# Optimization experiments

Measured on AMD Instinct MI355X. Metric: run time of the kernel, lower is better.

The kernel has to match this reference:

```python
import jax, jax.numpy as jnp
import numpy as np

B, S, D = 2, 2048, 1024
H = 16
DK = D // H
SCALE = 1.0 / np.sqrt(DK)

def setup_inputs() -> dict:
    key = jax.random.key(0)
    ks = jax.random.split(key, 11)
    std = 1.0 / np.sqrt(D)
    return {
        "query": jax.random.normal(ks[0], (B, S, D), jnp.float32),
        "key":   jax.random.normal(ks[1], (B, S, D), jnp.float32),
        "value": jax.random.normal(ks[2], (B, S, D), jnp.float32),
        "Wq": jax.random.normal(ks[3], (D, H * DK), jnp.float32) * std,
        "bq": jnp.zeros((H * DK,), jnp.float32),
        "Wk": jax.random.normal(ks[4], (D, H * DK), jnp.float32) * std,
        "bk": jnp.zeros((H * DK,), jnp.float32),
        "Wv": jax.random.normal(ks[5], (D, H * DK), jnp.float32) * std,
        "bv": jnp.zeros((H * DK,), jnp.float32),
        "Wo": jax.random.normal(ks[6], (D, D), jnp.float32) * std,
        "bo": jnp.zeros((D,), jnp.float32),
    }

def reference(query, key, value, Wq, bq, Wk, bk, Wv, bv, Wo, bo):
    b, s, _ = query.shape
    # projections -> [b, s, h, d_k]
    q = (query @ Wq + bq).reshape(b, s, H, DK)
    k = (key   @ Wk + bk).reshape(b, s, H, DK)
    v = (value @ Wv + bv).reshape(b, s, H, DK)
    # scores [b, i, j, h]
    scores = jnp.einsum('bihd,bjhd->bijh', q, k) * SCALE
    attn = jax.nn.softmax(scores, axis=2)  # softmax over key dim j
    # dropout rate 0.0 (eval mode) -> identity
    x = jnp.einsum('bijh,bjhd->bihd', attn, v).reshape(b, s, H * DK)
    return x @ Wo + bo
```

## Files before the change

### kernel.cpp

```cpp
#include <hip/hip_runtime.h>
#include <hip/hip_bf16.h>
#include <math.h>
#include <stdint.h>

constexpr int Bb = 2, Ss = 2048, Dd = 1024, Hh = 16;
constexpr int Mm = Bb * Ss;
constexpr int Nn = Dd;
constexpr int Kk = Dd;
constexpr float QSCALE = 0.125f * 1.44269504088896340736f;

typedef unsigned short ushort_t;
typedef __attribute__((ext_vector_type(8))) short bf16x8;
typedef __attribute__((ext_vector_type(4))) float f32x4;

#if __has_builtin(__builtin_amdgcn_exp2f)
#define EXP2F(x) __builtin_amdgcn_exp2f(x)
#else
#define EXP2F(x) exp2f(x)
#endif

__device__ __forceinline__ ushort_t f2bf(float f) {
  union { float f; unsigned u; } v; v.f = f;
  return (ushort_t)((v.u + 0x7fff + ((v.u >> 16) & 1)) >> 16);
}

__device__ __forceinline__ void load16_lds(const void* g, void* l) {
  __builtin_amdgcn_global_load_lds(
      (const __attribute__((address_space(1))) void*)(uintptr_t)g,
      (__attribute__((address_space(3))) void*)(uint32_t)(uintptr_t)l, 16, 0, 0);
}

__global__ __launch_bounds__(256) void prep(
    const float* __restrict__ q, const float* __restrict__ k,
    const float* __restrict__ v, ushort_t* __restrict__ qkvb,
    const float* __restrict__ Wq, const float* __restrict__ Wk,
    const float* __restrict__ Wv, const float* __restrict__ Wo,
    ushort_t* __restrict__ Wt) {
  const int bid = blockIdx.x;
  const int tid = threadIdx.x;
  if (bid < 12288) {
    const int z = bid >> 12, xi = bid & 4095;
    const float* src = (z == 0) ? q : (z == 1) ? k : v;
    ushort_t* dst = qkvb + (size_t)z * Mm * Kk;
    const size_t idx = ((size_t)xi * 256 + tid) * 4;
    const float4 val = *(const float4*)(src + idx);
    ushort4 o;
    o.x = f2bf(val.x); o.y = f2bf(val.y); o.z = f2bf(val.z); o.w = f2bf(val.w);
    *(ushort4*)(dst + idx) = o;
    return;
  }
  const int bid2 = bid - 12288;
  const int z = bid2 >> 8, rem = bid2 & 255;
  const float* W = (z == 0) ? Wq : (z == 1) ? Wk : (z == 2) ? Wv : Wo;
  ushort_t* out = Wt + (size_t)z * Kk * Nn;
  __shared__ float t[64][65];
  const int n0 = (rem & 15) * 64, k0 = (rem >> 4) * 64;
  const int lr = tid >> 4, lc = (tid & 15) * 4;
#pragma unroll
  for (int i = 0; i < 4; i++) {
    const int r = lr + i * 16;
    const float4 vv = *(const float4*)(W + (size_t)(k0 + r) * Nn + n0 + lc);
    t[r][lc] = vv.x; t[r][lc + 1] = vv.y; t[r][lc + 2] = vv.z; t[r][lc + 3] = vv.w;
  }
  __syncthreads();
  const int n = tid >> 2, kc = (tid & 3) * 16;
  ushort_t tmp[16];
#pragma unroll
  for (int j = 0; j < 16; j++) tmp[j] = f2bf(t[kc + j][n]);
  ushort_t* op = out + (size_t)(n0 + n) * Kk + k0 + kc;
  ((uint4*)op)[0] = ((uint4*)tmp)[0];
  ((uint4*)op)[1] = ((uint4*)tmp)[1];
}

__global__ __launch_bounds__(256) void transpose_v(
    const ushort_t* __restrict__ Vp, ushort_t* __restrict__ Vt) {
  __shared__ ushort_t t[64][68];
  const int tid = threadIdx.x;
  const int s0 = blockIdx.x * 64, h = blockIdx.y, b = blockIdx.z;
  const int lr = tid >> 4, lc = (tid & 15) * 4;
#pragma unroll
  for (int i = 0; i < 4; i++) {
    const int r = lr + i * 16;
    const ushort4 v =
        *(const ushort4*)(Vp + (size_t)(b * Ss + s0 + r) * Dd + h * 64 + lc);
    *(ushort4*)&t[r][lc] = v;
  }
  __syncthreads();
  const int d = tid >> 2, sc = (tid & 3) * 16;
  ushort_t tmp[16];
#pragma unroll
  for (int j = 0; j < 16; j++) tmp[j] = t[sc + j][d];
  ushort_t* op = Vt + ((size_t)b * Dd + h * 64 + d) * Ss + s0 + sc;
  ((uint4*)op)[0] = ((uint4*)tmp)[0];
  ((uint4*)op)[1] = ((uint4*)tmp)[1];
}

template <int BN, bool OUT_BF16>
__global__ __launch_bounds__(256) void gemm_mfma(
    const ushort_t* __restrict__ Abase, size_t a_stride,
    const ushort_t* __restrict__ Wbase, size_t w_stride,
    const float* __restrict__ bias0, const float* __restrict__ bias1,
    const float* __restrict__ bias2, void* __restrict__ Cbase, size_t c_stride,
    float scale_z0) {
  constexpr int BM = 128, BK = 32;
  constexpr int WM = (BN == 128) ? 64 : 32;
  constexpr int MT_ = WM / 16, NT_ = 4;
  __shared__ ushort_t As[BM * BK];
  __shared__ ushort_t Bs[BN * BK];
  const int tid = threadIdx.x, lane = tid & 63, wid = tid >> 6;
  const int z = blockIdx.z;
  const ushort_t* A = Abase + (size_t)z * a_stride;
  const ushort_t* Wt = Wbase + (size_t)z * w_stride;
  const float* bias = (z == 0) ? bias0 : (z == 1) ? bias1 : bias2;
  const float sc = (z == 0) ? scale_z0 : 1.0f;
  const int m0 = blockIdx.y * BM, n0 = blockIdx.x * BN;
  const int wm = (BN == 128) ? (wid >> 1) * 64 : wid * 32;
  const int wn = (BN == 128) ? (wid & 1) * 64 : 0;
  const int quad = lane >> 4, r16 = lane & 15;
  const int srow = lane >> 2;
  const int scol = (lane & 3) * 8;

  f32x4 acc[MT_][NT_];
#pragma unroll
  for (int m = 0; m < MT_; m++)
#pragma unroll
    for (int n = 0; n < NT_; n++) acc[m][n] = f32x4{0.f, 0.f, 0.f, 0.f};

  for (int k0 = 0; k0 < Kk; k0 += BK) {
    __syncthreads();
#pragma unroll
    for (int i = 0; i < BM / 64; i++) {
      const int I = wid * (BM / 64) + i;
      load16_lds(A + (size_t)(m0 + I * 16 + srow) * Kk + k0 + scol, As + I * 512);
    }
#pragma unroll
    for (int i = 0; i < BN / 64; i++) {
      const int I = wid * (BN / 64) + i;
      load16_lds(Wt + (size_t)(n0 + I * 16 + srow) * Kk + k0 + scol, Bs + I * 512);
    }
    __syncthreads();
    bf16x8 af[MT_], bfr[NT_];
#pragma unroll
    for (int m = 0; m < MT_; m++)
      af[m] = *(const bf16x8*)(As + (wm + m * 16 + r16) * BK + quad * 8);
#pragma unroll
    for (int n = 0; n < NT_; n++)
      bfr[n] = *(const bf16x8*)(Bs + (wn + n * 16 + r16) * BK + quad * 8);
#pragma unroll
    for (int m = 0; m < MT_; m++)
#pragma unroll
      for (int n = 0; n < NT_; n++)
        acc[m][n] =
            __builtin_amdgcn_mfma_f32_16x16x32_bf16(af[m], bfr[n], acc[m][n], 0, 0, 0);
  }

#pragma unroll
  for (int m = 0; m < MT_; m++) {
#pragma unroll
    for (int n = 0; n < NT_; n++) {
      const int gc = n0 + wn + n * 16 + r16;
      const float bv = bias[gc];
#pragma unroll
      for (int r = 0; r < 4; r++) {
        const int gr = m0 + wm + m * 16 + quad * 4 + r;
        const float v = (acc[m][n][r] + bv) * sc;
        if (OUT_BF16)
          ((ushort_t*)Cbase)[(size_t)z * c_stride + (size_t)gr * Nn + gc] = f2bf(v);
        else
          ((float*)Cbase)[(size_t)z * c_stride + (size_t)gr * Nn + gc] = v;
      }
    }
  }
}

__global__ __launch_bounds__(256) void flash_mfma(
    const ushort_t* __restrict__ Qp, const ushort_t* __restrict__ Kp,
    const ushort_t* __restrict__ Vt, ushort_t* __restrict__ Xp) {
  __shared__ ushort_t Ks[2][64 * 64];
  __shared__ ushort_t Vts[2][64 * 64];
  __shared__ ushort_t Ps[64 * 64];
  const int tid = threadIdx.x, lane = tid & 63, wid = tid >> 6;
  const int lid = blockIdx.x + (blockIdx.y << 5) + (blockIdx.z << 9);
  const int swzb = ((lid & 7) << 7) + (lid >> 3);
  const int qt = swzb & 31, h = (swzb >> 5) & 15, b = swzb >> 9;
  const int quad = lane >> 4, r16 = lane & 15;
  const int row8 = lane >> 3;
  const int colsw = ((lane & 7) ^ (row8 & 7)) * 8;
  const int swz = r16 & 7;
  const int psw2 = (r16 & 7) * 2;

  const int qrow = wid * 16 + r16;
  const ushort_t* Qg = Qp + ((size_t)(b * Ss + qt * 64)) * Dd + h * 64;
  const ushort_t* Kg = Kp + ((size_t)b * Ss) * Dd + h * 64;
  const ushort_t* Vg = Vt + ((size_t)b * Dd + h * 64) * Ss;

  bf16x8 qf[2];
#pragma unroll
  for (int ks = 0; ks < 2; ks++)
    qf[ks] = *(const bf16x8*)(Qg + (size_t)qrow * Dd + ks * 32 + quad * 8);

  f32x4 acc[4];
  float rs = 0.f;
#pragma unroll
  for (int mt = 0; mt < 4; mt++) acc[mt] = f32x4{0.f, 0.f, 0.f, 0.f};

  auto stage = [&](int kt, int bsel) {
#pragma unroll
    for (int i = 0; i < 2; i++) {
      const int I = wid * 2 + i;
      load16_lds(Kg + (size_t)(kt * 64 + I * 8 + row8) * Dd + colsw,
                 &Ks[bsel][I * 512]);
      load16_lds(Vg + (size_t)(I * 8 + row8) * Ss + kt * 64 + colsw,
                 &Vts[bsel][I * 512]);
    }
  };

  stage(0, 0);
  asm volatile("s_waitcnt vmcnt(4)" ::: "memory");

  for (int kt = 0; kt < Ss / 64; kt++) {
    const int cur = kt & 1;
    if (kt + 1 < Ss / 64) {
      stage(kt + 1, cur ^ 1);
      asm volatile("s_waitcnt vmcnt(4)\n\ts_barrier" ::: "memory");
    } else {
      asm volatile("s_waitcnt vmcnt(0)\n\ts_barrier" ::: "memory");
    }

    f32x4 sacc[4];
#pragma unroll
    for (int mm = 0; mm < 4; mm++) sacc[mm] = f32x4{0.f, 0.f, 0.f, 0.f};
    __builtin_amdgcn_s_setprio(1);
#pragma unroll
    for (int ks = 0; ks < 2; ks++) {
      const int ko = ((ks * 4 + quad) ^ swz) * 8;
      bf16x8 kf[4];
#pragma unroll
      for (int mm = 0; mm < 4; mm++)
        kf[mm] = *(const bf16x8*)(&Ks[cur][(mm * 16 + r16) * 64 + ko]);
#pragma unroll
      for (int mm = 0; mm < 4; mm++)
        sacc[mm] = __builtin_amdgcn_mfma_f32_16x16x32_bf16(
            kf[mm], qf[ks], sacc[mm], 0, 0, 0);
    }
    __builtin_amdgcn_s_setprio(0);

#pragma unroll
    for (int mm = 0; mm < 4; mm++) {
      float p0 = EXP2F(sacc[mm][0]), p1 = EXP2F(sacc[mm][1]);
      float p2 = EXP2F(sacc[mm][2]), p3 = EXP2F(sacc[mm][3]);
      rs += (p0 + p1) + (p2 + p3);
      union { __hip_bfloat162 hh; unsigned u; } lo, hi;
      lo.hh = __float22bfloat162_rn(make_float2(p0, p1));
      hi.hh = __float22bfloat162_rn(make_float2(p2, p3));
      *(uint2*)(Ps + qrow * 64 + (((mm * 4 + quad) ^ psw2) << 2)) =
          make_uint2(lo.u, hi.u);
    }

    __builtin_amdgcn_s_setprio(1);
#pragma unroll
    for (int ks = 0; ks < 2; ks++) {
      const int ko = ((ks * 4 + quad) ^ swz) * 8;
      bf16x8 vf[4];
#pragma unroll
      for (int mt = 0; mt < 4; mt++)
        vf[mt] = *(const bf16x8*)(&Vts[cur][(mt * 16 + r16) * 64 + ko]);
      const bf16x8 pf = *(const bf16x8*)(
          Ps + qrow * 64 + ((((ks * 4 + quad) << 1) ^ psw2) << 2));
#pragma unroll
      for (int mt = 0; mt < 4; mt++)
        acc[mt] = __builtin_amdgcn_mfma_f32_16x16x32_bf16(
            vf[mt], pf, acc[mt], 0, 0, 0);
    }
    __builtin_amdgcn_s_setprio(0);

    asm volatile("s_barrier" ::: "memory");
  }

  rs += __shfl_xor(rs, 16, 64);
  rs += __shfl_xor(rs, 32, 64);
  const float inv = 1.0f / rs;

#pragma unroll
  for (int mt = 0; mt < 4; mt++) {
    ushort4 o;
    o.x = f2bf(acc[mt][0] * inv);
    o.y = f2bf(acc[mt][1] * inv);
    o.z = f2bf(acc[mt][2] * inv);
    o.w = f2bf(acc[mt][3] * inv);
    *(ushort4*)(Xp + (size_t)(b * Ss + qt * 64 + qrow) * Dd +
                h * 64 + mt * 16 + quad * 4) = o;
  }
}

extern "C" void kernel_launch(void* const* d_in, const int* in_sizes, int n_in,
                              void* d_out, int out_size, void* d_ws,
                              size_t ws_size, hipStream_t stream) {
  const float* q  = (const float*)d_in[0];
  const float* k  = (const float*)d_in[1];
  const float* v  = (const float*)d_in[2];
  const float* Wq = (const float*)d_in[3];
  const float* bq = (const float*)d_in[4];
  const float* Wk = (const float*)d_in[5];
  const float* bk = (const float*)d_in[6];
  const float* Wv = (const float*)d_in[7];
  const float* bv = (const float*)d_in[8];
  const float* Wo = (const float*)d_in[9];
  const float* bo = (const float*)d_in[10];

  ushort_t* ws = (ushort_t*)d_ws;
  const size_t MD = (size_t)Mm * Kk;
  const size_t KN = (size_t)Kk * Nn;
  ushort_t* qkvb = ws;
  ushort_t* Wt   = ws + 3 * MD;
  ushort_t* QKVp = Wt + 4 * KN;
  ushort_t* Vtp  = QKVp + 3 * MD;
  ushort_t* Xp   = qkvb;

  prep<<<dim3(13312), 256, 0, stream>>>(q, k, v, qkvb, Wq, Wk, Wv, Wo, Wt);
  gemm_mfma<128, true><<<dim3(Nn / 128, Mm / 128, 3), 256, 0, stream>>>(
      qkvb, MD, Wt, KN, bq, bk, bv, QKVp, MD, QSCALE);
  transpose_v<<<dim3(Ss / 64, Hh, Bb), 256, 0, stream>>>(QKVp + 2 * MD, Vtp);
  flash_mfma<<<dim3(Ss / 64, Hh, Bb), 256, 0, stream>>>(QKVp, QKVp + MD, Vtp, Xp);
  gemm_mfma<64, false><<<dim3(Nn / 64, Mm / 128, 1), 256, 0, stream>>>(
      Xp, 0, Wt + 3 * KN, 0, bo, bo, bo, d_out, 0, 1.0f);
}
```

Before: 239.1 us.

## Split attention key dimension across waves and keep P in registers

Reorganises the flash attention kernel so each wave handles all 64 query rows for its own 16-key slice of every key tile, instead of 16 query rows over all keys. The exp'd probabilities feed straight into 16x16x16 MFMAs from registers, removing the LDS round trip for the P tile. The four waves' partial output accumulators and row sums are then reduced through shared memory at the end. This raises per-wave accumulator register use and adds an epilogue reduction with several barriers, and it sets a launch-bounds occupancy hint of three blocks.

```diff
diff --git a/kernel.cpp b/kernel.cpp
--- a/kernel.cpp
+++ b/kernel.cpp
@@ -11,6 +11,7 @@
 
 typedef unsigned short ushort_t;
 typedef __attribute__((ext_vector_type(8))) short bf16x8;
+typedef __attribute__((ext_vector_type(4))) short bf16x4;
 typedef __attribute__((ext_vector_type(4))) float f32x4;
 
 #if __has_builtin(__builtin_amdgcn_exp2f)
@@ -22,6 +23,15 @@
 __device__ __forceinline__ ushort_t f2bf(float f) {
   union { float f; unsigned u; } v; v.f = f;
   return (ushort_t)((v.u + 0x7fff + ((v.u >> 16) & 1)) >> 16);
+}
+
+__device__ __forceinline__ f32x4 mfma16(bf16x4 a, bf16x4 b, f32x4 c) {
+#if __has_builtin(__builtin_amdgcn_mfma_f32_16x16x16bf16_1k)
+  return __builtin_amdgcn_mfma_f32_16x16x16bf16_1k(a, b, c, 0, 0, 0);
+#else
+  asm("v_mfma_f32_16x16x16_bf16 %0, %1, %2, %0" : "+v"(c) : "v"(a), "v"(b));
+  return c;
+#endif
 }
 
 __device__ __forceinline__ void load16_lds(const void* g, void* l) {
@@ -173,45 +183,54 @@
   }
 }
 
-__global__ __launch_bounds__(256) void flash_mfma(
+__global__ __launch_bounds__(256, 3) void flash_mfma(
     const ushort_t* __restrict__ Qp, const ushort_t* __restrict__ Kp,
     const ushort_t* __restrict__ Vt, ushort_t* __restrict__ Xp) {
-  __shared__ ushort_t Ks[2][64 * 64];
-  __shared__ ushort_t Vts[2][64 * 64];
-  __shared__ ushort_t Ps[64 * 64];
+  __shared__ __align__(16) char smem[2 * 64 * 68 * 4];
+  ushort_t* KsU = (ushort_t*)smem;
+  ushort_t* VtsU = KsU + 2 * 4096;
+
   const int tid = threadIdx.x, lane = tid & 63, wid = tid >> 6;
   const int lid = blockIdx.x + (blockIdx.y << 5) + (blockIdx.z << 9);
   const int swzb = ((lid & 7) << 7) + (lid >> 3);
   const int qt = swzb & 31, h = (swzb >> 5) & 15, b = swzb >> 9;
   const int quad = lane >> 4, r16 = lane & 15;
   const int row8 = lane >> 3;
-  const int colsw = ((lane & 7) ^ (row8 & 7)) * 8;
+  const int colsw = ((lane & 7) ^ row8) * 8;
   const int swz = r16 & 7;
-  const int psw2 = (r16 & 7) * 2;
-
-  const int qrow = wid * 16 + r16;
+
   const ushort_t* Qg = Qp + ((size_t)(b * Ss + qt * 64)) * Dd + h * 64;
   const ushort_t* Kg = Kp + ((size_t)b * Ss) * Dd + h * 64;
   const ushort_t* Vg = Vt + ((size_t)b * Dd + h * 64) * Ss;
 
-  bf16x8 qf[2];
-#pragma unroll
-  for (int ks = 0; ks < 2; ks++)
-    qf[ks] = *(const bf16x8*)(Qg + (size_t)qrow * Dd + ks * 32 + quad * 8);
-
-  f32x4 acc[4];
-  float rs = 0.f;
-#pragma unroll
-  for (int mt = 0; mt < 4; mt++) acc[mt] = f32x4{0.f, 0.f, 0.f, 0.f};
+  bf16x8 qf[2][4];
+#pragma unroll
+  for (int n = 0; n < 4; n++)
+#pragma unroll
+    for (int ks = 0; ks < 2; ks++)
+      qf[ks][n] = *(const bf16x8*)(Qg + (size_t)(n * 16 + r16) * Dd + ks * 32 + quad * 8);
+
+  const uint32_t kbase = (uint32_t)(wid * 16 + r16) * 64;
+  const uint32_t koff0 = kbase + (uint32_t)(((0 * 4 + quad) ^ swz) << 3);
+  const uint32_t koff1 = kbase + (uint32_t)(((1 * 4 + quad) ^ swz) << 3);
+  const int vG = wid * 2 + (quad >> 1);
+  const uint32_t vcol = (uint32_t)(((vG ^ swz) << 3) + (quad & 1) * 4);
+
+  f32x4 acc[4][4];
+#pragma unroll
+  for (int mt = 0; mt < 4; mt++)
+#pragma unroll
+    for (int n = 0; n < 4; n++) acc[mt][n] = f32x4{0.f, 0.f, 0.f, 0.f};
+  float rsn[4] = {0.f, 0.f, 0.f, 0.f};
 
   auto stage = [&](int kt, int bsel) {
 #pragma unroll
     for (int i = 0; i < 2; i++) {
       const int I = wid * 2 + i;
       load16_lds(Kg + (size_t)(kt * 64 + I * 8 + row8) * Dd + colsw,
-                 &Ks[bsel][I * 512]);
+                 KsU + bsel * 4096 + I * 512);
       load16_lds(Vg + (size_t)(I * 8 + row8) * Ss + kt * 64 + colsw,
-                 &Vts[bsel][I * 512]);
+                 VtsU + bsel * 4096 + I * 512);
     }
   };
 
@@ -226,70 +245,116 @@
     } else {
       asm volatile("s_waitcnt vmcnt(0)\n\ts_barrier" ::: "memory");
     }
-
+    const ushort_t* Kc = KsU + cur * 4096;
+    const ushort_t* Vc = VtsU + cur * 4096;
+
+    const bf16x8 kf0 = *(const bf16x8*)(Kc + koff0);
+    const bf16x8 kf1 = *(const bf16x8*)(Kc + koff1);
     f32x4 sacc[4];
 #pragma unroll
-    for (int mm = 0; mm < 4; mm++) sacc[mm] = f32x4{0.f, 0.f, 0.f, 0.f};
+    for (int n = 0; n < 4; n++) sacc[n] = f32x4{0.f, 0.f, 0.f, 0.f};
     __builtin_amdgcn_s_setprio(1);
 #pragma unroll
-    for (int ks = 0; ks < 2; ks++) {
-      const int ko = ((ks * 4 + quad) ^ swz) * 8;
-      bf16x8 kf[4];
-#pragma unroll
-      for (int mm = 0; mm < 4; mm++)
-        kf[mm] = *(const bf16x8*)(&Ks[cur][(mm * 16 + r16) * 64 + ko]);
-#pragma unroll
-      for (int mm = 0; mm < 4; mm++)
-        sacc[mm] = __builtin_amdgcn_mfma_f32_16x16x32_bf16(
-            kf[mm], qf[ks], sacc[mm], 0, 0, 0);
-    }
+    for (int n = 0; n < 4; n++)
+      sacc[n] = __builtin_amdgcn_mfma_f32_16x16x32_bf16(kf0, qf[0][n], sacc[n], 0, 0, 0);
+#pragma unroll
+    for (int n = 0; n < 4; n++)
+      sacc[n] = __builtin_amdgcn_mfma_f32_16x16x32_bf16(kf1, qf[1][n], sacc[n], 0, 0, 0);
     __builtin_amdgcn_s_setprio(0);
 
-#pragma unroll
-    for (int mm = 0; mm < 4; mm++) {
-      float p0 = EXP2F(sacc[mm][0]), p1 = EXP2F(sacc[mm][1]);
-      float p2 = EXP2F(sacc[mm][2]), p3 = EXP2F(sacc[mm][3]);
-      rs += (p0 + p1) + (p2 + p3);
+    bf16x4 pf[4];
+#pragma unroll
+    for (int n = 0; n < 4; n++) {
+      const float p0 = EXP2F(sacc[n][0]), p1 = EXP2F(sacc[n][1]);
+      const float p2 = EXP2F(sacc[n][2]), p3 = EXP2F(sacc[n][3]);
+      rsn[n] += (p0 + p1) + (p2 + p3);
       union { __hip_bfloat162 hh; unsigned u; } lo, hi;
       lo.hh = __float22bfloat162_rn(make_float2(p0, p1));
       hi.hh = __float22bfloat162_rn(make_float2(p2, p3));
-      *(uint2*)(Ps + qrow * 64 + (((mm * 4 + quad) ^ psw2) << 2)) =
-          make_uint2(lo.u, hi.u);
-    }
-
+      union { uint2 u2; bf16x4 v; } pk;
+      pk.u2 = make_uint2(lo.u, hi.u);
+      pf[n] = pk.v;
+    }
+
+    bf16x4 vf[4];
+#pragma unroll
+    for (int mt = 0; mt < 4; mt++)
+      vf[mt] = *(const bf16x4*)(Vc + (uint32_t)(mt * 16 + r16) * 64 + vcol);
     __builtin_amdgcn_s_setprio(1);
 #pragma unroll
-    for (int ks = 0; ks < 2; ks++) {
-      const int ko = ((ks * 4 + quad) ^ swz) * 8;
-      bf16x8 vf[4];
-#pragma unroll
-      for (int mt = 0; mt < 4; mt++)
-        vf[mt] = *(const bf16x8*)(&Vts[cur][(mt * 16 + r16) * 64 + ko]);
-      const bf16x8 pf = *(const bf16x8*)(
-          Ps + qrow * 64 + ((((ks * 4 + quad) << 1) ^ psw2) << 2));
-#pragma unroll
-      for (int mt = 0; mt < 4; mt++)
-        acc[mt] = __builtin_amdgcn_mfma_f32_16x16x32_bf16(
-            vf[mt], pf, acc[mt], 0, 0, 0);
-    }
+    for (int mt = 0; mt < 4; mt++)
+#pragma unroll
+      for (int n = 0; n < 4; n++)
+        acc[mt][n] = mfma16(vf[mt], pf[n], acc[mt][n]);
     __builtin_amdgcn_s_setprio(0);
 
     asm volatile("s_barrier" ::: "memory");
   }
 
-  rs += __shfl_xor(rs, 16, 64);
-  rs += __shfl_xor(rs, 32, 64);
-  const float inv = 1.0f / rs;
-
-#pragma unroll
-  for (int mt = 0; mt < 4; mt++) {
-    ushort4 o;
-    o.x = f2bf(acc[mt][0] * inv);
-    o.y = f2bf(acc[mt][1] * inv);
-    o.z = f2bf(acc[mt][2] * inv);
-    o.w = f2bf(acc[mt][3] * inv);
-    *(ushort4*)(Xp + (size_t)(b * Ss + qt * 64 + qrow) * Dd +
-                h * 64 + mt * 16 + quad * 4) = o;
+#pragma unroll
+  for (int n = 0; n < 4; n++) {
+    float r = rsn[n];
+    r += __shfl_xor(r, 16, 64);
+    r += __shfl_xor(r, 32, 64);
+    rsn[n] = r;
+  }
+
+  float* red = (float*)smem;
+  __syncthreads();
+  if (wid & 2) {
+    float* p = red + (size_t)(wid & 1) * (64 * 68) + (size_t)lane * 68;
+#pragma unroll
+    for (int mt = 0; mt < 4; mt++)
+#pragma unroll
+      for (int n = 0; n < 4; n++)
+        *(f32x4*)(p + (mt * 4 + n) * 4) = acc[mt][n];
+    p[64] = rsn[0]; p[65] = rsn[1]; p[66] = rsn[2]; p[67] = rsn[3];
+  }
+  __syncthreads();
+  if (!(wid & 2)) {
+    const float* p = red + (size_t)wid * (64 * 68) + (size_t)lane * 68;
+#pragma unroll
+    for (int mt = 0; mt < 4; mt++)
+#pragma unroll
+      for (int n = 0; n < 4; n++)
+        acc[mt][n] += *(const f32x4*)(p + (mt * 4 + n) * 4);
+    rsn[0] += p[64]; rsn[1] += p[65]; rsn[2] += p[66]; rsn[3] += p[67];
+  }
+  __syncthreads();
+  if (wid == 1) {
+    float* p = red + (size_t)lane * 68;
+#pragma unroll
+    for (int mt = 0; mt < 4; mt++)
+#pragma unroll
+      for (int n = 0; n < 4; n++)
+        *(f32x4*)(p + (mt * 4 + n) * 4) = acc[mt][n];
+    p[64] = rsn[0]; p[65] = rsn[1]; p[66] = rsn[2]; p[67] = rsn[3];
+  }
+  __syncthreads();
+  if (wid == 0) {
+    const float* p = red + (size_t)lane * 68;
+#pragma unroll
+    for (int mt = 0; mt < 4; mt++)
+#pragma unroll
+      for (int n = 0; n < 4; n++)
+        acc[mt][n] += *(const f32x4*)(p + (mt * 4 + n) * 4);
+    rsn[0] += p[64]; rsn[1] += p[65]; rsn[2] += p[66]; rsn[3] += p[67];
+    float inv[4];
+#pragma unroll
+    for (int n = 0; n < 4; n++) inv[n] = 1.0f / rsn[n];
+#pragma unroll
+    for (int mt = 0; mt < 4; mt++) {
+#pragma unroll
+      for (int n = 0; n < 4; n++) {
+        ushort4 o;
+        o.x = f2bf(acc[mt][n][0] * inv[n]);
+        o.y = f2bf(acc[mt][n][1] * inv[n]);
+        o.z = f2bf(acc[mt][n][2] * inv[n]);
+        o.w = f2bf(acc[mt][n][3] * inv[n]);
+        *(ushort4*)(Xp + (size_t)(b * Ss + qt * 64 + n * 16 + r16) * Dd +
+                    h * 64 + mt * 16 + quad * 4) = o;
+      }
+    }
   }
 }
 
```

Result: no change. 237.3 us (-0.7%).
